# Optimization experiments

Hardware: AMD Instinct MI355X
Metric: run time of the kernel (lower is better)

Reference implementation:

```python
import jax, jax.numpy as jnp
import numpy as np

D_MODEL = 1024
N_HEADS = 16
HEAD_DIM = D_MODEL // N_HEADS


def setup_inputs() -> dict:
    key = jax.random.key(0)
    k1, k2, k3 = jax.random.split(key, 3)
    B, S = 4, 2048
    x = jax.random.normal(k1, (B, S, D_MODEL), dtype=jnp.float32)
    # scaled init so logits stay reasonable
    w_qkv = jax.random.normal(k2, (D_MODEL, 3 * D_MODEL), dtype=jnp.float32) / np.sqrt(D_MODEL)
    b_qkv = jnp.zeros((3 * D_MODEL,), dtype=jnp.float32)
    w_out = jax.random.normal(k3, (D_MODEL, D_MODEL), dtype=jnp.float32) / np.sqrt(D_MODEL)
    b_out = jnp.zeros((D_MODEL,), dtype=jnp.float32)
    return {"x": x, "w_qkv": w_qkv, "b_qkv": b_qkv, "w_out": w_out, "b_out": b_out}


def reference(x, w_qkv, b_qkv, w_out, b_out):
    B, S, D = x.shape
    qkv = x @ w_qkv + b_qkv                      # [B,S,3D]
    q, k, v = jnp.split(qkv, 3, axis=-1)
    def split_heads(t):
        return t.reshape(B, S, N_HEADS, HEAD_DIM).transpose(0, 2, 1, 3)  # [B,H,S,d]
    q, k, v = split_heads(q), split_heads(k), split_heads(v)
    a = jnp.einsum('bhsd,bhtd->bhst', q, k)      # [B,H,S,S]
    # causal mask added BEFORE scaling, as in the original module
    causal_mask = jnp.triu(jnp.full((S, S), -jnp.inf, dtype=a.dtype), k=1)
    a = (a + causal_mask) / np.sqrt(HEAD_DIM)
    a = jax.nn.softmax(a, axis=-1)
    z = jnp.einsum('bhst,bhtd->bhsd', a, v)      # [B,H,S,d]
    z = z.transpose(0, 2, 1, 3).reshape(B, S, D)
    return z @ w_out + b_out
```

## Files before the change

### kernel.cpp

```cpp
#include <hip/hip_runtime.h>
#include <hip/hip_bf16.h>
#include <stdint.h>

#define B_   4
#define S_   2048
#define H_   16
#define HD_  64
#define D_   1024

typedef short  short8  __attribute__((ext_vector_type(8)));
typedef float  f32x4   __attribute__((ext_vector_type(4)));
typedef float  f32x16  __attribute__((ext_vector_type(16)));

__device__ __forceinline__ unsigned short f2bf(float f) {
    union { float f; unsigned u; } v; v.f = f;
    unsigned r = v.u + 0x7fffu + ((v.u >> 16) & 1u);
    return (unsigned short)(r >> 16);
}

#if __has_builtin(__builtin_amdgcn_exp2f)
#define EXP2(x) __builtin_amdgcn_exp2f(x)
#else
#define EXP2(x) exp2f(x)
#endif

__device__ __forceinline__ unsigned cvtpk(float lo, float hi) {
    unsigned r;
    asm("v_cvt_pk_bf16_f32 %0, %1, %2" : "=v"(r) : "v"(lo), "v"(hi));
    return r;
}

__device__ __forceinline__ float bq(float v, int srclane) {
    return __int_as_float(__builtin_amdgcn_ds_bpermute(srclane << 2, __float_as_int(v)));
}

__device__ __forceinline__ void pl32swap(unsigned &x, unsigned &y) {
    asm volatile("v_permlane32_swap_b32 %0, %1" : "+v"(x), "+v"(y));
}

#define MFMA32(a, b, c) __builtin_amdgcn_mfma_f32_32x32x16_bf16(a, b, c, 0, 0, 0)

__global__ __launch_bounds__(256) void k_cvt(const float* __restrict__ in,
                                             unsigned short* __restrict__ out) {
    int i = (blockIdx.x * 256 + threadIdx.x) * 4;
    float4 f = *(const float4*)(in + i);
    ushort4 o;
    o.x = f2bf(f.x); o.y = f2bf(f.y); o.z = f2bf(f.z); o.w = f2bf(f.w);
    *(ushort4*)(out + i) = o;
}

__global__ __launch_bounds__(256) void k_transpose_cvt(const float* __restrict__ in,
                                                       unsigned short* __restrict__ out,
                                                       int K, int N) {
    __shared__ float tile[32][33];
    int n0 = blockIdx.x * 32, k0 = blockIdx.y * 32;
    int tx = threadIdx.x, ty = threadIdx.y;
#pragma unroll
    for (int i = 0; i < 32; i += 8)
        tile[ty + i][tx] = in[(size_t)(k0 + ty + i) * N + n0 + tx];
    __syncthreads();
#pragma unroll
    for (int i = 0; i < 32; i += 8)
        out[(size_t)(n0 + ty + i) * K + k0 + tx] = f2bf(tile[tx][ty + i]);
}

__device__ __forceinline__ void async_load16(const unsigned short* g, unsigned short* l) {
    __builtin_amdgcn_global_load_lds(
        (const __attribute__((address_space(1))) unsigned int*)g,
        (__attribute__((address_space(3))) unsigned int*)l, 16, 0, 0);
}

template <int EPI>
__global__ __launch_bounds__(256) void k_gemm(const unsigned short* __restrict__ A,
                                              const unsigned short* __restrict__ BT,
                                              const float* __restrict__ bias,
                                              float* __restrict__ outf,
                                              unsigned short* __restrict__ qb,
                                              unsigned short* __restrict__ kb,
                                              unsigned short* __restrict__ vtb,
                                              int M, int N, int K) {
    __shared__ __attribute__((aligned(16))) unsigned short As[128 * 64];
    __shared__ __attribute__((aligned(16))) unsigned short Bs[128 * 64];
    const int tid = threadIdx.x, wave = tid >> 6, lane = tid & 63;
    const int m0 = blockIdx.y * 128, n0 = blockIdx.x * 128;
    const int wr = wave >> 1, wc = wave & 1;

    f32x4 acc[4][4] = {};

    for (int kt = 0; kt < K; kt += 64) {
#pragma unroll
        for (int p = 0; p < 4; p++) {
            int bu = p * 256 + wave * 64;
            int u0 = bu + lane;
            int row = u0 >> 3;
            int col8 = (u0 & 7) ^ (row & 7);
            async_load16(A  + (size_t)(m0 + row) * K + kt + col8 * 8, As + bu * 8);
            async_load16(BT + (size_t)(n0 + row) * K + kt + col8 * 8, Bs + bu * 8);
        }
        __syncthreads();
#pragma unroll
        for (int kk = 0; kk < 2; kk++) {
            short8 af[4], bf[4];
#pragma unroll
            for (int i = 0; i < 4; i++) {
                int ra = wr * 64 + i * 16 + (lane & 15);
                int rb = wc * 64 + i * 16 + (lane & 15);
                int cb = (kk * 32 + (lane >> 4) * 8) * 2;
                af[i] = *(const short8*)((const char*)As + ra * 128 + (cb ^ ((ra & 7) << 4)));
                bf[i] = *(const short8*)((const char*)Bs + rb * 128 + (cb ^ ((rb & 7) << 4)));
            }
#pragma unroll
            for (int i = 0; i < 4; i++)
#pragma unroll
                for (int j = 0; j < 4; j++)
                    acc[i][j] = __builtin_amdgcn_mfma_f32_16x16x32_bf16(af[i], bf[j], acc[i][j], 0, 0, 0);
        }
        __syncthreads();
    }

#pragma unroll
    for (int i = 0; i < 4; i++) {
#pragma unroll
        for (int j = 0; j < 4; j++) {
            int n = n0 + wc * 64 + j * 16 + (lane & 15);
            float bv = bias[n];
#pragma unroll
            for (int r = 0; r < 4; r++) {
                int m = m0 + wr * 64 + i * 16 + ((lane >> 4) << 2) + r;
                float val = acc[i][j][r] + bv;
                if (EPI == 0) {
                    int part = n >> 10, rem = n & 1023;
                    int h = rem >> 6, d = rem & 63;
                    int b = m >> 11, s = m & 2047;
                    size_t bh = (size_t)(b * 16 + h);
                    if (part == 2) {
                        size_t off = bh * 131072 +
                            (size_t)(((s >> 5) * 4) + (d >> 5) * 2 + ((s >> 4) & 1)) * 512 +
                            (((d & 31) << 1) + ((s >> 3) & 1)) * 8 + (s & 7);
                        vtb[off] = f2bf(val);
                    } else {
                        size_t off = bh * 131072 +
                            (size_t)(((s >> 5) * 4) + (d >> 4)) * 512 +
                            (((s & 31) << 1) + ((d >> 3) & 1)) * 8 + (d & 7);
                        if (part == 0) qb[off] = f2bf(val * 0.18033688011112042f);
                        else           kb[off] = f2bf(val);
                    }
                } else {
                    outf[(size_t)m * N + n] = val;
                }
            }
        }
    }
}

__device__ __forceinline__ void do_strip(int strip, int bh, int c, int hi,
                                         const unsigned short* __restrict__ QFb,
                                         const unsigned short* __restrict__ KFb,
                                         const unsigned short* __restrict__ VFb,
                                         unsigned short* __restrict__ Z) {
    const int qbase = strip * 32;
    const int b = bh >> 4, h = bh & 15;
    const int lp8 = ((c << 1) + hi) << 3;

    short8 qf[4];
#pragma unroll
    for (int kd = 0; kd < 4; kd++)
        qf[kd] = *(const short8*)(QFb + (strip * 4 + kd) * 512 + lp8);

    f32x16 o0a = {}, o0b = {}, o1a = {}, o1b = {};
    float l_r = 0.f;
    const int nkv = strip + 1;

    short8 kf_cur[4], kf_nxt[4];
#pragma unroll
    for (int kd = 0; kd < 4; kd++)
        kf_cur[kd] = *(const short8*)(KFb + kd * 512 + lp8);

    for (int tt = 0; tt < nkv; ++tt) {
        const int tn = (tt + 1 < nkv) ? (tt + 1) : tt;
#pragma unroll
        for (int kd = 0; kd < 4; kd++)
            kf_nxt[kd] = *(const short8*)(KFb + (tn * 4 + kd) * 512 + lp8);

        short8 vf[2][2];
#pragma unroll
        for (int dt = 0; dt < 2; dt++)
#pragma unroll
            for (int ks = 0; ks < 2; ks++)
                vf[dt][ks] = *(const short8*)(VFb + (tt * 4 + dt * 2 + ks) * 512 + lp8);

        f32x16 sTa = {}, sTb = {};
        sTa = MFMA32(kf_cur[0], qf[0], sTa);
        sTb = MFMA32(kf_cur[2], qf[2], sTb);
        sTa = MFMA32(kf_cur[1], qf[1], sTa);
        sTb = MFMA32(kf_cur[3], qf[3], sTb);
        f32x16 sT;
#pragma unroll
        for (int r = 0; r < 16; r++) sT[r] = sTa[r] + sTb[r];

        if (tt * 32 == qbase) {
#pragma unroll
            for (int r = 0; r < 16; r++) {
                int tl = (r & 3) + 8 * (r >> 2) + 4 * hi;
                if (tl > c) sT[r] = -1e30f;
            }
        }

#pragma unroll
        for (int r = 0; r < 16; r++) sT[r] = EXP2(sT[r]);
        float s0 = sT[0] + sT[8],  s1 = sT[1] + sT[9];
        float s2 = sT[2] + sT[10], s3 = sT[3] + sT[11];
        float s4 = sT[4] + sT[12], s5 = sT[5] + sT[13];
        float s6 = sT[6] + sT[14], s7 = sT[7] + sT[15];
        s0 += s4; s1 += s5; s2 += s6; s3 += s7;
        l_r += (s0 + s2) + (s1 + s3);

        unsigned pk0 = cvtpk(sT[0],  sT[1]);
        unsigned pk1 = cvtpk(sT[2],  sT[3]);
        unsigned pk2 = cvtpk(sT[4],  sT[5]);
        unsigned pk3 = cvtpk(sT[6],  sT[7]);
        unsigned pk4 = cvtpk(sT[8],  sT[9]);
        unsigned pk5 = cvtpk(sT[10], sT[11]);
        unsigned pk6 = cvtpk(sT[12], sT[13]);
        unsigned pk7 = cvtpk(sT[14], sT[15]);
        pl32swap(pk0, pk2);
        pl32swap(pk1, pk3);
        pl32swap(pk4, pk6);
        pl32swap(pk5, pk7);
        union { unsigned u[4]; short8 s; } pa0, pa1;
        pa0.u[0] = pk0; pa0.u[1] = pk1; pa0.u[2] = pk2; pa0.u[3] = pk3;
        pa1.u[0] = pk4; pa1.u[1] = pk5; pa1.u[2] = pk6; pa1.u[3] = pk7;

        o0a = MFMA32(pa0.s, vf[0][0], o0a);
        o1a = MFMA32(pa0.s, vf[1][0], o1a);
        o0b = MFMA32(pa1.s, vf[0][1], o0b);
        o1b = MFMA32(pa1.s, vf[1][1], o1b);

#pragma unroll
        for (int kd = 0; kd < 4; kd++) kf_cur[kd] = kf_nxt[kd];
    }

    l_r += __shfl_xor(l_r, 32);
    float inv = __builtin_amdgcn_rcpf(l_r);
#pragma unroll
    for (int r = 0; r < 16; r++) {
        int crow = (r & 3) + 8 * (r >> 2) + 4 * hi;
        float ib = bq(inv, crow);
        int q = qbase + crow;
        unsigned short* zp = Z + ((size_t)b * S_ + q) * D_ + h * HD_;
        zp[c]      = f2bf((o0a[r] + o0b[r]) * ib);
        zp[32 + c] = f2bf((o1a[r] + o1b[r]) * ib);
    }
}

__global__ __launch_bounds__(64, 2) void k_attn(const unsigned short* __restrict__ QF,
                                                const unsigned short* __restrict__ KF,
                                                const unsigned short* __restrict__ VF,
                                                unsigned short* __restrict__ Z) {
    const int i = blockIdx.x;
    const int bh = (i & 7) * 8 + ((i >> 3) & 7);
    const int pr = i >> 6;
    const int lane = threadIdx.x & 63;
    const int c = lane & 31, hi = lane >> 5;
    const unsigned short* QFb = QF + (size_t)bh * 131072;
    const unsigned short* KFb = KF + (size_t)bh * 131072;
    const unsigned short* VFb = VF + (size_t)bh * 131072;
    do_strip(pr,      bh, c, hi, QFb, KFb, VFb, Z);
    do_strip(63 - pr, bh, c, hi, QFb, KFb, VFb, Z);
}

extern "C" void kernel_launch(void* const* d_in, const int* in_sizes, int n_in,
                              void* d_out, int out_size, void* d_ws, size_t ws_size,
                              hipStream_t stream) {
    const float* x     = (const float*)d_in[0];
    const float* w_qkv = (const float*)d_in[1];
    const float* b_qkv = (const float*)d_in[2];
    const float* w_out = (const float*)d_in[3];
    const float* b_out = (const float*)d_in[4];
    float* out = (float*)d_out;

    char* ws = (char*)d_ws;
    unsigned short* xb    = (unsigned short*)(ws + 0);
    unsigned short* wqkvT = (unsigned short*)(ws + 16777216);
    unsigned short* woutT = (unsigned short*)(ws + 23068672);
    unsigned short* qb    = (unsigned short*)(ws + 25165824);
    unsigned short* kb    = (unsigned short*)(ws + 41943040);
    unsigned short* vtb   = (unsigned short*)(ws + 58720256);
    unsigned short* zb    = xb;

    k_cvt<<<8192, 256, 0, stream>>>(x, xb);
    k_transpose_cvt<<<dim3(96, 32), dim3(32, 8), 0, stream>>>(w_qkv, wqkvT, 1024, 3072);
    k_transpose_cvt<<<dim3(32, 32), dim3(32, 8), 0, stream>>>(w_out, woutT, 1024, 1024);
    k_gemm<0><<<dim3(24, 64), 256, 0, stream>>>(xb, wqkvT, b_qkv, nullptr, qb, kb, vtb,
                                                8192, 3072, 1024);
    k_attn<<<2048, 64, 0, stream>>>(qb, kb, vtb, zb);
    k_gemm<1><<<dim3(8, 64), 256, 0, stream>>>(zb, woutT, b_out, out, nullptr, nullptr, nullptr,
                                               8192, 1024, 1024);
}
```

Before: 195.2 us.

## Double-buffer GEMM LDS tiles, swizzle block order for XCDs, raise MFMA priority

The GEMM kernel now keeps two LDS buffers and issues the async global-to-LDS loads for the next K tile before computing the current one, so memory latency can overlap with MFMA work. The grid becomes 1D with a remap that groups consecutive tiles per XCD (blockIdx & 7), aiming for better L2 reuse, and s_setprio is raised around the MFMA burst. LDS use per block doubles to 64 KB, which may lower occupancy.

```diff
diff --git a/kernel.cpp b/kernel.cpp
--- a/kernel.cpp
+++ b/kernel.cpp
@@ -78,45 +78,73 @@
                                               unsigned short* __restrict__ qb,
                                               unsigned short* __restrict__ kb,
                                               unsigned short* __restrict__ vtb,
-                                              int M, int N, int K) {
-    __shared__ __attribute__((aligned(16))) unsigned short As[128 * 64];
-    __shared__ __attribute__((aligned(16))) unsigned short Bs[128 * 64];
+                                              int M, int N, int K, int nbx) {
+    __shared__ __attribute__((aligned(16))) unsigned short As0[128 * 64];
+    __shared__ __attribute__((aligned(16))) unsigned short Bs0[128 * 64];
+    __shared__ __attribute__((aligned(16))) unsigned short As1[128 * 64];
+    __shared__ __attribute__((aligned(16))) unsigned short Bs1[128 * 64];
     const int tid = threadIdx.x, wave = tid >> 6, lane = tid & 63;
-    const int m0 = blockIdx.y * 128, n0 = blockIdx.x * 128;
+    const int nwg = nbx * (M >> 7);
+    const int cpx = nwg >> 3;
+    const int swz = (blockIdx.x & 7) * cpx + (blockIdx.x >> 3);
+    const int m0 = (swz % (M >> 7)) * 128, n0 = (swz / (M >> 7)) * 128;
     const int wr = wave >> 1, wc = wave & 1;
 
+    int srow[4], scol8[4], sbu[4];
+#pragma unroll
+    for (int p = 0; p < 4; p++) {
+        int bu = p * 256 + wave * 64;
+        int u0 = bu + lane;
+        sbu[p]   = bu * 8;
+        srow[p]  = u0 >> 3;
+        scol8[p] = ((u0 & 7) ^ (srow[p] & 7)) * 8;
+    }
+
+#define STAGE(AD, BD, KT)                                                           \
+    _Pragma("unroll")                                                               \
+    for (int p = 0; p < 4; p++) {                                                   \
+        async_load16(A  + (size_t)(m0 + srow[p]) * K + (KT) + scol8[p], AD + sbu[p]); \
+        async_load16(BT + (size_t)(n0 + srow[p]) * K + (KT) + scol8[p], BD + sbu[p]); \
+    }
+
     f32x4 acc[4][4] = {};
 
-    for (int kt = 0; kt < K; kt += 64) {
-#pragma unroll
-        for (int p = 0; p < 4; p++) {
-            int bu = p * 256 + wave * 64;
-            int u0 = bu + lane;
-            int row = u0 >> 3;
-            int col8 = (u0 & 7) ^ (row & 7);
-            async_load16(A  + (size_t)(m0 + row) * K + kt + col8 * 8, As + bu * 8);
-            async_load16(BT + (size_t)(n0 + row) * K + kt + col8 * 8, Bs + bu * 8);
+#define COMPUTE(AS, BS)                                                              \
+    _Pragma("unroll")                                                                \
+    for (int kk = 0; kk < 2; kk++) {                                                 \
+        short8 af[4], bf[4];                                                         \
+        _Pragma("unroll")                                                            \
+        for (int i = 0; i < 4; i++) {                                                \
+            int ra = wr * 64 + i * 16 + (lane & 15);                                 \
+            int rb = wc * 64 + i * 16 + (lane & 15);                                 \
+            int cb = (kk * 32 + (lane >> 4) * 8) * 2;                                \
+            af[i] = *(const short8*)((const char*)AS + ra * 128 + (cb ^ ((ra & 7) << 4))); \
+            bf[i] = *(const short8*)((const char*)BS + rb * 128 + (cb ^ ((rb & 7) << 4))); \
+        }                                                                            \
+        __builtin_amdgcn_s_setprio(1);                                               \
+        _Pragma("unroll")                                                            \
+        for (int i = 0; i < 4; i++)                                                  \
+            _Pragma("unroll")                                                        \
+            for (int j = 0; j < 4; j++)                                              \
+                acc[i][j] = __builtin_amdgcn_mfma_f32_16x16x32_bf16(af[i], bf[j], acc[i][j], 0, 0, 0); \
+        __builtin_amdgcn_s_setprio(0);                                               \
+    }
+
+    const int NT = K >> 6;
+    STAGE(As0, Bs0, 0)
+    __syncthreads();
+    for (int t = 0; t < NT; t += 2) {
+        if (t + 1 < NT) STAGE(As1, Bs1, (t + 1) * 64)
+        COMPUTE(As0, Bs0)
+        __syncthreads();
+        if (t + 2 < NT) STAGE(As0, Bs0, (t + 2) * 64)
+        if (t + 1 < NT) {
+            COMPUTE(As1, Bs1)
+            __syncthreads();
         }
-        __syncthreads();
-#pragma unroll
-        for (int kk = 0; kk < 2; kk++) {
-            short8 af[4], bf[4];
-#pragma unroll
-            for (int i = 0; i < 4; i++) {
-                int ra = wr * 64 + i * 16 + (lane & 15);
-                int rb = wc * 64 + i * 16 + (lane & 15);
-                int cb = (kk * 32 + (lane >> 4) * 8) * 2;
-                af[i] = *(const short8*)((const char*)As + ra * 128 + (cb ^ ((ra & 7) << 4)));
-                bf[i] = *(const short8*)((const char*)Bs + rb * 128 + (cb ^ ((rb & 7) << 4)));
-            }
-#pragma unroll
-            for (int i = 0; i < 4; i++)
-#pragma unroll
-                for (int j = 0; j < 4; j++)
-                    acc[i][j] = __builtin_amdgcn_mfma_f32_16x16x32_bf16(af[i], bf[j], acc[i][j], 0, 0, 0);
-        }
-        __syncthreads();
-    }
+    }
+#undef STAGE
+#undef COMPUTE
 
 #pragma unroll
     for (int i = 0; i < 4; i++) {
@@ -291,9 +319,9 @@
     k_cvt<<<8192, 256, 0, stream>>>(x, xb);
     k_transpose_cvt<<<dim3(96, 32), dim3(32, 8), 0, stream>>>(w_qkv, wqkvT, 1024, 3072);
     k_transpose_cvt<<<dim3(32, 32), dim3(32, 8), 0, stream>>>(w_out, woutT, 1024, 1024);
-    k_gemm<0><<<dim3(24, 64), 256, 0, stream>>>(xb, wqkvT, b_qkv, nullptr, qb, kb, vtb,
-                                                8192, 3072, 1024);
+    k_gemm<0><<<1536, 256, 0, stream>>>(xb, wqkvT, b_qkv, nullptr, qb, kb, vtb,
+                                        8192, 3072, 1024, 24);
     k_attn<<<2048, 64, 0, stream>>>(qb, kb, vtb, zb);
-    k_gemm<1><<<dim3(8, 64), 256, 0, stream>>>(zb, woutT, b_out, out, nullptr, nullptr, nullptr,
-                                               8192, 1024, 1024);
-}
+    k_gemm<1><<<512, 256, 0, stream>>>(zb, woutT, b_out, out, nullptr, nullptr, nullptr,
+                                       8192, 1024, 1024, 8);
+}
```

Result: slower. 203.4 us (+4.2%).
